# Optimization experiments

Measured on AMD Instinct MI355X. Metric: run time of the kernel, lower is better.

Reference implementation:

```python
import jax, jax.numpy as jnp
import numpy as np

H, D = 16, 64          # num_heads, head_dim
OUT = H * D            # out_dim = 1024
W1, W2 = 32, 32        # sliding windows
EPS_NORM = 1e-7
EPS_LN = 1e-5


def setup_inputs() -> dict:
    key = jax.random.key(0)
    ks = jax.random.split(key, 6)
    B, S, IN = 2, 2048, 1024
    x = jax.random.normal(ks[0], (B, S, IN), dtype=jnp.float32)
    scale = 0.02
    W_Q = jax.random.normal(ks[1], (IN, OUT), dtype=jnp.float32) * scale
    W_K = jax.random.normal(ks[2], (IN, OUT), dtype=jnp.float32) * scale
    W_V = jax.random.normal(ks[3], (IN, OUT), dtype=jnp.float32) * scale
    W_Kp = jax.random.normal(ks[4], (IN, OUT), dtype=jnp.float32) * scale
    W_O = jax.random.normal(ks[5], (OUT, OUT), dtype=jnp.float32) * scale
    ln_gamma = jnp.ones((OUT,), dtype=jnp.float32)
    ln_beta = jnp.zeros((OUT,), dtype=jnp.float32)
    return {"x": x, "W_Q": W_Q, "W_K": W_K, "W_V": W_V, "W_Kp": W_Kp,
            "W_O": W_O, "ln_gamma": ln_gamma, "ln_beta": ln_beta}


def _l2norm(t):
    return t / (jnp.linalg.norm(t, axis=-1, keepdims=True) + EPS_NORM)


def reference(x, W_Q, W_K, W_V, W_Kp, W_O, ln_gamma, ln_beta):
    B, S, _ = x.shape
    # projections -> (B, S, H, D)
    Q = _l2norm((x @ W_Q).reshape(B, S, H, D))
    K = _l2norm((x @ W_K).reshape(B, S, H, D))
    Kp = _l2norm((x @ W_Kp).reshape(B, S, H, D))
    V = (x @ W_V).reshape(B, S, H, D)
    # windowed keys/values (last w1/w2 positions, as in the PyTorch fallback)
    K_win = K[:, -W1:]
    Kp_win = Kp[:, -W2:]
    V_win = V[:, -W1:]
    Vp_win = V[:, -W2:]
    # triple product A_ijk = q.k.k' / sqrt(D) -> (B, S, H, w1, w2)
    A = jnp.einsum('bshd,bjhd,bkhd->bshjk', Q, K_win, Kp_win) / jnp.sqrt(jnp.float32(D))
    # causal window mask: allow j <= i + w1 - S and k <= i + w2 - S
    s_idx = jnp.arange(S)[:, None, None]
    j_idx = jnp.arange(W1)[None, :, None]
    k_idx = jnp.arange(W2)[None, None, :]
    mask = (j_idx > s_idx + (W1 - S)) | (k_idx > s_idx + (W2 - S))  # (S, w1, w2)
    neg_inf = jnp.float32(-jnp.inf)
    A = jnp.where(mask[None, :, None, :, :], neg_inf, A)
    # joint softmax over (j, k); fully-masked query rows produce zeros
    A_flat = A.reshape(B, S, H, W1 * W2)
    all_masked = jnp.all(A_flat == neg_inf, axis=-1, keepdims=True)
    A_safe = jnp.where(all_masked, 0.0, A_flat)
    P = jax.nn.softmax(A_safe, axis=-1)
    P = jnp.where(all_masked, 0.0, P).reshape(B, S, H, W1, W2)
    # value outer-product weighting (V' = V)
    Z = jnp.einsum('bshjk,bjhd,bkhd->bshd', P, V_win, Vp_win)
    out = Z.reshape(B, S, OUT) @ W_O
    out = out + x  # residual (shapes match)
    # LayerNorm
    mu = jnp.mean(out, axis=-1, keepdims=True)
    var = jnp.mean((out - mu) ** 2, axis=-1, keepdims=True)
    out = (out - mu) / jnp.sqrt(var + EPS_LN) * ln_gamma + ln_beta
    return out
```

## Files before the change

kernel.cpp:

```cpp
#include <hip/hip_runtime.h>
#include <math.h>


#define XS 68
#define WS 68

#define YP_STR   262144
#define NKS_P    8
#define ZF_OFF   (NKS_P * YP_STR)
#define DP_OFF   (ZF_OFF + 65536)
#define DP_STR   65536
#define NKS_W    16

__device__ __forceinline__ void ln_row(
    const float4* __restrict__ x4, const float4* __restrict__ g4,
    const float4* __restrict__ b4, float4* __restrict__ out4,
    int row, int lane) {
  float4 v[4];
  #pragma unroll
  for (int i = 0; i < 4; i++) v[i] = x4[row * 256 + i * 64 + lane];
  float sum = 0.f, ss = 0.f;
  #pragma unroll
  for (int i = 0; i < 4; i++) {
    sum += v[i].x + v[i].y + v[i].z + v[i].w;
    ss  += v[i].x * v[i].x + v[i].y * v[i].y + v[i].z * v[i].z + v[i].w * v[i].w;
  }
  #pragma unroll
  for (int off = 1; off < 64; off <<= 1) {
    sum += __shfl_xor(sum, off);
    ss  += __shfl_xor(ss, off);
  }
  float mu   = sum * (1.f / 1024.f);
  float rstd = rsqrtf(ss * (1.f / 1024.f) - mu * mu + 1e-5f);
  #pragma unroll
  for (int i = 0; i < 4; i++) {
    float4 g  = g4[i * 64 + lane];
    float4 be = b4[i * 64 + lane];
    float4 o;
    o.x = (v[i].x - mu) * rstd * g.x + be.x;
    o.y = (v[i].y - mu) * rstd * g.y + be.y;
    o.z = (v[i].z - mu) * rstd * g.z + be.z;
    o.w = (v[i].w - mu) * rstd * g.w + be.w;
    out4[row * 256 + i * 64 + lane] = o;
  }
}

__global__ __launch_bounds__(256, 4) void proj_ln_kernel(
    const float* __restrict__ x,
    const float* __restrict__ Wq, const float* __restrict__ Wk,
    const float* __restrict__ Wkp, const float* __restrict__ Wv,
    const float* __restrict__ gam, const float* __restrict__ bet,
    float* __restrict__ Y, float* __restrict__ out) {
  __shared__ float xs[64 * WS];
  __shared__ float wl[64 * WS];
  const int tid = threadIdx.x;
  const int bid = blockIdx.x;

  if (bid < 512) {
    const int cb   = bid & 63;
    const int ks   = bid >> 6;
    const int col0 = cb * 64;
    const int z    = cb >> 4;
    const int colz = col0 & 1023;
    const float* __restrict__ W =
        (z == 0) ? Wq : ((z == 1) ? Wk : ((z == 2) ? Wkp : Wv));
    const int tc = tid & 15, tr = tid >> 4;

    float acc[4][4];
    #pragma unroll
    for (int i = 0; i < 4; i++)
      #pragma unroll
      for (int j = 0; j < 4; j++) acc[i][j] = 0.f;

    for (int cc = 0; cc < 2; cc++) {
      const int kb = ks * 128 + cc * 64;
      #pragma unroll
      for (int i = 0; i < 4; i++) {
        int e = i * 256 + tid;
        int r = e >> 4, q = e & 15;
        int b = r >> 5, t = r & 31;
        float4 v = *(const float4*)(x + ((b * 2048 + 2016 + t) * 1024 + kb + q * 4));
        xs[(q * 4 + 0) * WS + r] = v.x;
        xs[(q * 4 + 1) * WS + r] = v.y;
        xs[(q * 4 + 2) * WS + r] = v.z;
        xs[(q * 4 + 3) * WS + r] = v.w;
        float4 w = *(const float4*)(W + (size_t)(kb + r) * 1024 + colz + q * 4);
        *(float4*)(wl + r * WS + q * 4) = w;
      }
      __syncthreads();

      #pragma unroll 8
      for (int kk = 0; kk < 64; kk++) {
        float4 xv = *(const float4*)(xs + kk * WS + tr * 4);
        float4 wv = *(const float4*)(wl + kk * WS + tc * 4);
        acc[0][0] = fmaf(xv.x, wv.x, acc[0][0]);
        acc[0][1] = fmaf(xv.x, wv.y, acc[0][1]);
        acc[0][2] = fmaf(xv.x, wv.z, acc[0][2]);
        acc[0][3] = fmaf(xv.x, wv.w, acc[0][3]);
        acc[1][0] = fmaf(xv.y, wv.x, acc[1][0]);
        acc[1][1] = fmaf(xv.y, wv.y, acc[1][1]);
        acc[1][2] = fmaf(xv.y, wv.z, acc[1][2]);
        acc[1][3] = fmaf(xv.y, wv.w, acc[1][3]);
        acc[2][0] = fmaf(xv.z, wv.x, acc[2][0]);
        acc[2][1] = fmaf(xv.z, wv.y, acc[2][1]);
        acc[2][2] = fmaf(xv.z, wv.z, acc[2][2]);
        acc[2][3] = fmaf(xv.z, wv.w, acc[2][3]);
        acc[3][0] = fmaf(xv.w, wv.x, acc[3][0]);
        acc[3][1] = fmaf(xv.w, wv.y, acc[3][1]);
        acc[3][2] = fmaf(xv.w, wv.z, acc[3][2]);
        acc[3][3] = fmaf(xv.w, wv.w, acc[3][3]);
      }
      __syncthreads();
    }

    float* __restrict__ Yo = Y + ks * YP_STR + col0;
    #pragma unroll
    for (int i = 0; i < 4; i++) {
      float4 o = make_float4(acc[i][0], acc[i][1], acc[i][2], acc[i][3]);
      *(float4*)(Yo + (tr * 4 + i) * 4096 + tc * 4) = o;
    }
  } else {
    const int wave = tid >> 6, lane = tid & 63;
    const int gw = (bid - 512) * 4 + wave;
    const float4* x4 = (const float4*)x;
    const float4* g4 = (const float4*)gam;
    const float4* b4 = (const float4*)bet;
    float4* out4 = (float4*)out;
    for (int idx = gw; idx < 4032; idx += 1792) {
      int row = (idx < 2016) ? idx : idx + 32;
      ln_row(x4, g4, b4, out4, row, lane);
    }
  }
}

__global__ __launch_bounds__(256) void attn_kernel(
    const float* __restrict__ Y, float* __restrict__ Zout) {
  __shared__ float Kn[32 * XS], Kp[32 * XS], Vs[32 * XS];
  __shared__ float Pt[4][32 * 33];
  __shared__ float qs[4][64];
  const int tid = threadIdx.x;
  const int wave = tid >> 6, lane = tid & 63;
  const int h = blockIdx.y, b = blockIdx.z;

  #pragma unroll
  for (int i = 0; i < 8; i++) {
    int e = i * 256 + tid;
    int row = e >> 6, d = e & 63;
    int src = (b * 32 + row) * 4096 + h * 64 + d;
    float kn = 0.f, kp = 0.f, vv = 0.f;
    #pragma unroll
    for (int p = 0; p < NKS_P; p++) {
      const float* Yp = Y + p * YP_STR + src;
      kn += Yp[1024]; kp += Yp[2048]; vv += Yp[3072];
    }
    Kn[row * XS + d] = kn; Kp[row * XS + d] = kp; Vs[row * XS + d] = vv;
  }
  __syncthreads();

  for (int rr = 0; rr < 8; rr++) {
    int row = wave * 8 + rr;
    float kv = Kn[row * XS + lane];
    float s2 = kv * kv;
    #pragma unroll
    for (int off = 1; off < 64; off <<= 1) s2 += __shfl_xor(s2, off);
    Kn[row * XS + lane] = kv * (1.f / (sqrtf(s2) + 1e-7f));
    float pv = Kp[row * XS + lane];
    float p2 = pv * pv;
    #pragma unroll
    for (int off = 1; off < 64; off <<= 1) p2 += __shfl_xor(p2, off);
    Kp[row * XS + lane] = pv * (1.f / (sqrtf(p2) + 1e-7f));
  }
  __syncthreads();

  const int m = blockIdx.x * 4 + wave;
  const int r = b * 32 + m;

  float q = 0.f;
  #pragma unroll
  for (int p = 0; p < NKS_P; p++) q += Y[p * YP_STR + r * 4096 + h * 64 + lane];
  float q2 = q * q;
  #pragma unroll
  for (int off = 1; off < 64; off <<= 1) q2 += __shfl_xor(q2, off);
  q *= (1.f / (sqrtf(q2) + 1e-7f));
  qs[wave][lane] = q;
  __builtin_amdgcn_wave_barrier();

  const int lj = lane >> 3, lk = lane & 7;
  float acc[4][4];
  #pragma unroll
  for (int a = 0; a < 4; a++)
    #pragma unroll
    for (int c = 0; c < 4; c++) acc[a][c] = 0.f;

  const float* qw = qs[wave];
  for (int dq = 0; dq < 16; dq++) {
    float4 q4 = *(const float4*)(qw + dq * 4);
    float4 t4[4], kp4[4];
    #pragma unroll
    for (int tj = 0; tj < 4; tj++) {
      float4 kv = *(const float4*)(Kn + (lj * 4 + tj) * XS + dq * 4);
      t4[tj].x = q4.x * kv.x; t4[tj].y = q4.y * kv.y;
      t4[tj].z = q4.z * kv.z; t4[tj].w = q4.w * kv.w;
    }
    #pragma unroll
    for (int tk = 0; tk < 4; tk++)
      kp4[tk] = *(const float4*)(Kp + (lk * 4 + tk) * XS + dq * 4);
    #pragma unroll
    for (int tj = 0; tj < 4; tj++)
      #pragma unroll
      for (int tk = 0; tk < 4; tk++)
        acc[tj][tk] += t4[tj].x * kp4[tk].x + t4[tj].y * kp4[tk].y
                     + t4[tj].z * kp4[tk].z + t4[tj].w * kp4[tk].w;
  }

  float amax = -1e30f;
  #pragma unroll
  for (int tj = 0; tj < 4; tj++)
    #pragma unroll
    for (int tk = 0; tk < 4; tk++) {
      int j = lj * 4 + tj, k = lk * 4 + tk;
      if (j <= m && k <= m) amax = fmaxf(amax, acc[tj][tk] * 0.125f);
    }
  #pragma unroll
  for (int off = 1; off < 64; off <<= 1) amax = fmaxf(amax, __shfl_xor(amax, off));

  float lsum = 0.f;
  float* ptw = Pt[wave];
  #pragma unroll
  for (int tj = 0; tj < 4; tj++)
    #pragma unroll
    for (int tk = 0; tk < 4; tk++) {
      int j = lj * 4 + tj, k = lk * 4 + tk;
      float e = 0.f;
      if (j <= m && k <= m) e = __expf(acc[tj][tk] * 0.125f - amax);
      lsum += e;
      ptw[k * 33 + j] = e;
    }
  #pragma unroll
  for (int off = 1; off < 64; off <<= 1) lsum += __shfl_xor(lsum, off);
  float inv = 1.f / lsum;
  __builtin_amdgcn_wave_barrier();

  float vreg[32];
  #pragma unroll
  for (int k = 0; k < 32; k++) vreg[k] = Vs[k * XS + lane];
  float zacc = 0.f;
  for (int k = 0; k <= m; k++) {
    float g = 0.f;
    #pragma unroll
    for (int j = 0; j < 32; j++) g += ptw[k * 33 + j] * vreg[j];
    zacc += g * vreg[k];
  }
  Zout[r * 1024 + h * 64 + lane] = zacc * inv;
}

__global__ __launch_bounds__(256, 4) void wo_kernel(
    const float* __restrict__ Zr, const float* __restrict__ Wo,
    float* __restrict__ Dp) {
  __shared__ float zs[64 * WS];
  __shared__ float wl[64 * WS];
  const int tid  = threadIdx.x;
  const int col0 = blockIdx.x * 64;
  const int ks   = blockIdx.y;
  const int kb   = ks * 64;
  const int tc = tid & 15, tr = tid >> 4;

  #pragma unroll
  for (int i = 0; i < 4; i++) {
    int e = i * 256 + tid;
    int r = e >> 4, q = e & 15;
    float4 v = *(const float4*)(Zr + r * 1024 + kb + q * 4);
    zs[(q * 4 + 0) * WS + r] = v.x;
    zs[(q * 4 + 1) * WS + r] = v.y;
    zs[(q * 4 + 2) * WS + r] = v.z;
    zs[(q * 4 + 3) * WS + r] = v.w;
    float4 w = *(const float4*)(Wo + (size_t)(kb + r) * 1024 + col0 + q * 4);
    *(float4*)(wl + r * WS + q * 4) = w;
  }
  __syncthreads();

  float acc[4][4];
  #pragma unroll
  for (int i = 0; i < 4; i++)
    #pragma unroll
    for (int j = 0; j < 4; j++) acc[i][j] = 0.f;

  #pragma unroll 8
  for (int kk = 0; kk < 64; kk++) {
    float4 xv = *(const float4*)(zs + kk * WS + tr * 4);
    float4 wv = *(const float4*)(wl + kk * WS + tc * 4);
    acc[0][0] = fmaf(xv.x, wv.x, acc[0][0]);
    acc[0][1] = fmaf(xv.x, wv.y, acc[0][1]);
    acc[0][2] = fmaf(xv.x, wv.z, acc[0][2]);
    acc[0][3] = fmaf(xv.x, wv.w, acc[0][3]);
    acc[1][0] = fmaf(xv.y, wv.x, acc[1][0]);
    acc[1][1] = fmaf(xv.y, wv.y, acc[1][1]);
    acc[1][2] = fmaf(xv.y, wv.z, acc[1][2]);
    acc[1][3] = fmaf(xv.y, wv.w, acc[1][3]);
    acc[2][0] = fmaf(xv.z, wv.x, acc[2][0]);
    acc[2][1] = fmaf(xv.z, wv.y, acc[2][1]);
    acc[2][2] = fmaf(xv.z, wv.z, acc[2][2]);
    acc[2][3] = fmaf(xv.z, wv.w, acc[2][3]);
    acc[3][0] = fmaf(xv.w, wv.x, acc[3][0]);
    acc[3][1] = fmaf(xv.w, wv.y, acc[3][1]);
    acc[3][2] = fmaf(xv.w, wv.z, acc[3][2]);
    acc[3][3] = fmaf(xv.w, wv.w, acc[3][3]);
  }

  float* __restrict__ D = Dp + ks * DP_STR + col0;
  #pragma unroll
  for (int i = 0; i < 4; i++) {
    float4 o = make_float4(acc[i][0], acc[i][1], acc[i][2], acc[i][3]);
    *(float4*)(D + (tr * 4 + i) * 1024 + tc * 4) = o;
  }
}

__global__ __launch_bounds__(256, 4) void ln_win_kernel(
    const float4* __restrict__ x4, const float4* __restrict__ dp4,
    const float4* __restrict__ g4, const float4* __restrict__ b4,
    float4* __restrict__ out4) {
  const int tid = threadIdx.x;
  const int wave = tid >> 6, lane = tid & 63;
  const int wr  = blockIdx.x * 4 + wave;
  const int row = (wr >> 5) * 2048 + 2016 + (wr & 31);

  float4 v[4];
  #pragma unroll
  for (int i = 0; i < 4; i++) v[i] = x4[row * 256 + i * 64 + lane];
  #pragma unroll
  for (int p = 0; p < NKS_W; p++) {
    #pragma unroll
    for (int i = 0; i < 4; i++) {
      float4 d = dp4[p * 16384 + wr * 256 + i * 64 + lane];
      v[i].x += d.x; v[i].y += d.y; v[i].z += d.z; v[i].w += d.w;
    }
  }
  float sum = 0.f, ss = 0.f;
  #pragma unroll
  for (int i = 0; i < 4; i++) {
    sum += v[i].x + v[i].y + v[i].z + v[i].w;
    ss  += v[i].x * v[i].x + v[i].y * v[i].y + v[i].z * v[i].z + v[i].w * v[i].w;
  }
  #pragma unroll
  for (int off = 1; off < 64; off <<= 1) {
    sum += __shfl_xor(sum, off);
    ss  += __shfl_xor(ss, off);
  }
  float mu   = sum * (1.f / 1024.f);
  float rstd = rsqrtf(ss * (1.f / 1024.f) - mu * mu + 1e-5f);

  #pragma unroll
  for (int i = 0; i < 4; i++) {
    float4 g = g4[i * 64 + lane];
    float4 be = b4[i * 64 + lane];
    float4 o;
    o.x = (v[i].x - mu) * rstd * g.x + be.x;
    o.y = (v[i].y - mu) * rstd * g.y + be.y;
    o.z = (v[i].z - mu) * rstd * g.z + be.z;
    o.w = (v[i].w - mu) * rstd * g.w + be.w;
    out4[row * 256 + i * 64 + lane] = o;
  }
}

extern "C" void kernel_launch(void* const* d_in, const int* in_sizes, int n_in,
                              void* d_out, int out_size, void* d_ws, size_t ws_size,
                              hipStream_t stream) {
  const float* x   = (const float*)d_in[0];
  const float* Wq  = (const float*)d_in[1];
  const float* Wk  = (const float*)d_in[2];
  const float* Wv  = (const float*)d_in[3];
  const float* Wkp = (const float*)d_in[4];
  const float* Wo  = (const float*)d_in[5];
  const float* gam = (const float*)d_in[6];
  const float* bet = (const float*)d_in[7];
  float* out = (float*)d_out;
  float* ws  = (float*)d_ws;

  hipLaunchKernelGGL(proj_ln_kernel, dim3(512 + 448), dim3(256), 0, stream,
                     x, Wq, Wk, Wkp, Wv, gam, bet, ws, out);
  hipLaunchKernelGGL(attn_kernel, dim3(8, 16, 2), dim3(256), 0, stream,
                     ws, ws + ZF_OFF);
  hipLaunchKernelGGL(wo_kernel, dim3(16, NKS_W), dim3(256), 0, stream,
                     ws + ZF_OFF, Wo, ws + DP_OFF);
  hipLaunchKernelGGL(ln_win_kernel, dim3(16), dim3(256), 0, stream,
                     (const float4*)x, (const float4*)(ws + DP_OFF),
                     (const float4*)gam, (const float4*)bet, (float4*)out);
}
```

Before: 128.8 us.

## Fuse attention, W_O projection and windowed LayerNorm into one kernel

Merges the attention, W_O matmul and window LayerNorm kernels into a single kernel. Each block multiplies its four Z rows for one head by that head's 64-row slice of W_O and writes per-head partial sums. The last block per row-group, found with an atomic counter and threadfence, sums the 16 partials and applies the residual and LayerNorm. This removes two kernel launches and the Z round trip through global memory. In exchange, W_O is read per block without shared-memory tiling, and the counters must be zeroed inside the projection kernel.

```diff
diff --git a/kernel.cpp b/kernel.cpp
--- a/kernel.cpp
+++ b/kernel.cpp
@@ -7,10 +7,9 @@
 
 #define YP_STR   262144
 #define NKS_P    8
-#define ZF_OFF   (NKS_P * YP_STR)
-#define DP_OFF   (ZF_OFF + 65536)
+#define DP_OFF   (NKS_P * YP_STR)
 #define DP_STR   65536
-#define NKS_W    16
+#define CNT_OFF  (DP_OFF + 16 * DP_STR)
 
 __device__ __forceinline__ void ln_row(
     const float4* __restrict__ x4, const float4* __restrict__ g4,
@@ -50,7 +49,7 @@
     const float* __restrict__ Wq, const float* __restrict__ Wk,
     const float* __restrict__ Wkp, const float* __restrict__ Wv,
     const float* __restrict__ gam, const float* __restrict__ bet,
-    float* __restrict__ Y, float* __restrict__ out) {
+    float* __restrict__ Y, float* __restrict__ out, int* __restrict__ cnt) {
   __shared__ float xs[64 * WS];
   __shared__ float wl[64 * WS];
   const int tid = threadIdx.x;
@@ -120,6 +119,7 @@
       *(float4*)(Yo + (tr * 4 + i) * 4096 + tc * 4) = o;
     }
   } else {
+    if (bid == 512 && tid < 16) cnt[tid] = 0;
     const int wave = tid >> 6, lane = tid & 63;
     const int gw = (bid - 512) * 4 + wave;
     const float4* x4 = (const float4*)x;
@@ -133,14 +133,19 @@
   }
 }
 
-__global__ __launch_bounds__(256) void attn_kernel(
-    const float* __restrict__ Y, float* __restrict__ Zout) {
+__global__ __launch_bounds__(256) void attn_wo_kernel(
+    const float* __restrict__ Y, const float* __restrict__ Wo,
+    const float* __restrict__ x, const float* __restrict__ gam,
+    const float* __restrict__ bet, float* __restrict__ Dp,
+    int* __restrict__ cnt, float* __restrict__ out) {
   __shared__ float Kn[32 * XS], Kp[32 * XS], Vs[32 * XS];
   __shared__ float Pt[4][32 * 33];
   __shared__ float qs[4][64];
+  __shared__ float Zs[4][64];
+  __shared__ int done_flag;
   const int tid = threadIdx.x;
   const int wave = tid >> 6, lane = tid & 63;
-  const int h = blockIdx.y, b = blockIdx.z;
+  const int mb = blockIdx.x, h = blockIdx.y, b = blockIdx.z;
 
   #pragma unroll
   for (int i = 0; i < 8; i++) {
@@ -172,7 +177,7 @@
   }
   __syncthreads();
 
-  const int m = blockIdx.x * 4 + wave;
+  const int m = mb * 4 + wave;
   const int r = b * 32 + m;
 
   float q = 0.f;
@@ -251,84 +256,59 @@
     for (int j = 0; j < 32; j++) g += ptw[k * 33 + j] * vreg[j];
     zacc += g * vreg[k];
   }
-  Zout[r * 1024 + h * 64 + lane] = zacc * inv;
-}
-
-__global__ __launch_bounds__(256, 4) void wo_kernel(
-    const float* __restrict__ Zr, const float* __restrict__ Wo,
-    float* __restrict__ Dp) {
-  __shared__ float zs[64 * WS];
-  __shared__ float wl[64 * WS];
-  const int tid  = threadIdx.x;
-  const int col0 = blockIdx.x * 64;
-  const int ks   = blockIdx.y;
-  const int kb   = ks * 64;
-  const int tc = tid & 15, tr = tid >> 4;
-
-  #pragma unroll
-  for (int i = 0; i < 4; i++) {
-    int e = i * 256 + tid;
-    int r = e >> 4, q = e & 15;
-    float4 v = *(const float4*)(Zr + r * 1024 + kb + q * 4);
-    zs[(q * 4 + 0) * WS + r] = v.x;
-    zs[(q * 4 + 1) * WS + r] = v.y;
-    zs[(q * 4 + 2) * WS + r] = v.z;
-    zs[(q * 4 + 3) * WS + r] = v.w;
-    float4 w = *(const float4*)(Wo + (size_t)(kb + r) * 1024 + col0 + q * 4);
-    *(float4*)(wl + r * WS + q * 4) = w;
-  }
-  __syncthreads();
-
-  float acc[4][4];
+  Zs[wave][lane] = zacc * inv;
+  __syncthreads();
+
+  float wacc[4][4];
   #pragma unroll
   for (int i = 0; i < 4; i++)
     #pragma unroll
-    for (int j = 0; j < 4; j++) acc[i][j] = 0.f;
-
-  #pragma unroll 8
-  for (int kk = 0; kk < 64; kk++) {
-    float4 xv = *(const float4*)(zs + kk * WS + tr * 4);
-    float4 wv = *(const float4*)(wl + kk * WS + tc * 4);
-    acc[0][0] = fmaf(xv.x, wv.x, acc[0][0]);
-    acc[0][1] = fmaf(xv.x, wv.y, acc[0][1]);
-    acc[0][2] = fmaf(xv.x, wv.z, acc[0][2]);
-    acc[0][3] = fmaf(xv.x, wv.w, acc[0][3]);
-    acc[1][0] = fmaf(xv.y, wv.x, acc[1][0]);
-    acc[1][1] = fmaf(xv.y, wv.y, acc[1][1]);
-    acc[1][2] = fmaf(xv.y, wv.z, acc[1][2]);
-    acc[1][3] = fmaf(xv.y, wv.w, acc[1][3]);
-    acc[2][0] = fmaf(xv.z, wv.x, acc[2][0]);
-    acc[2][1] = fmaf(xv.z, wv.y, acc[2][1]);
-    acc[2][2] = fmaf(xv.z, wv.z, acc[2][2]);
-    acc[2][3] = fmaf(xv.z, wv.w, acc[2][3]);
-    acc[3][0] = fmaf(xv.w, wv.x, acc[3][0]);
-    acc[3][1] = fmaf(xv.w, wv.y, acc[3][1]);
-    acc[3][2] = fmaf(xv.w, wv.z, acc[3][2]);
-    acc[3][3] = fmaf(xv.w, wv.w, acc[3][3]);
-  }
-
-  float* __restrict__ D = Dp + ks * DP_STR + col0;
-  #pragma unroll
-  for (int i = 0; i < 4; i++) {
-    float4 o = make_float4(acc[i][0], acc[i][1], acc[i][2], acc[i][3]);
-    *(float4*)(D + (tr * 4 + i) * 1024 + tc * 4) = o;
-  }
-}
-
-__global__ __launch_bounds__(256, 4) void ln_win_kernel(
-    const float4* __restrict__ x4, const float4* __restrict__ dp4,
-    const float4* __restrict__ g4, const float4* __restrict__ b4,
-    float4* __restrict__ out4) {
-  const int tid = threadIdx.x;
-  const int wave = tid >> 6, lane = tid & 63;
-  const int wr  = blockIdx.x * 4 + wave;
-  const int row = (wr >> 5) * 2048 + 2016 + (wr & 31);
+    for (int j = 0; j < 4; j++) wacc[i][j] = 0.f;
+
+  const float* __restrict__ WoS = Wo + (size_t)h * 65536 + tid * 4;
+  #pragma unroll 4
+  for (int k = 0; k < 64; k++) {
+    float4 wv = *(const float4*)(WoS + (size_t)k * 1024);
+    #pragma unroll
+    for (int rr = 0; rr < 4; rr++) {
+      float zz = Zs[rr][k];
+      wacc[rr][0] = fmaf(zz, wv.x, wacc[rr][0]);
+      wacc[rr][1] = fmaf(zz, wv.y, wacc[rr][1]);
+      wacc[rr][2] = fmaf(zz, wv.z, wacc[rr][2]);
+      wacc[rr][3] = fmaf(zz, wv.w, wacc[rr][3]);
+    }
+  }
+  const int r0 = b * 32 + mb * 4;
+  float* __restrict__ D = Dp + h * DP_STR;
+  #pragma unroll
+  for (int rr = 0; rr < 4; rr++) {
+    float4 o = make_float4(wacc[rr][0], wacc[rr][1], wacc[rr][2], wacc[rr][3]);
+    *(float4*)(D + (size_t)(r0 + rr) * 1024 + tid * 4) = o;
+  }
+
+  __threadfence();
+  __syncthreads();
+  if (tid == 0) {
+    int old = atomicAdd(cnt + (b * 8 + mb), 1);
+    done_flag = (old == 15) ? 1 : 0;
+  }
+  __syncthreads();
+  if (!done_flag) return;
+  __threadfence();
+
+  const int wr  = r0 + wave;
+  const int row = b * 2048 + 2016 + mb * 4 + wave;
+  const float4* x4  = (const float4*)x;
+  const float4* dp4 = (const float4*)Dp;
+  const float4* g4  = (const float4*)gam;
+  const float4* b4  = (const float4*)bet;
+  float4* out4 = (float4*)out;
 
   float4 v[4];
   #pragma unroll
   for (int i = 0; i < 4; i++) v[i] = x4[row * 256 + i * 64 + lane];
   #pragma unroll
-  for (int p = 0; p < NKS_W; p++) {
+  for (int p = 0; p < 16; p++) {
     #pragma unroll
     for (int i = 0; i < 4; i++) {
       float4 d = dp4[p * 16384 + wr * 256 + i * 64 + lane];
@@ -348,10 +328,9 @@
   }
   float mu   = sum * (1.f / 1024.f);
   float rstd = rsqrtf(ss * (1.f / 1024.f) - mu * mu + 1e-5f);
-
   #pragma unroll
   for (int i = 0; i < 4; i++) {
-    float4 g = g4[i * 64 + lane];
+    float4 g  = g4[i * 64 + lane];
     float4 be = b4[i * 64 + lane];
     float4 o;
     o.x = (v[i].x - mu) * rstd * g.x + be.x;
@@ -375,14 +354,10 @@
   const float* bet = (const float*)d_in[7];
   float* out = (float*)d_out;
   float* ws  = (float*)d_ws;
+  int*   cnt = (int*)(ws + CNT_OFF);
 
   hipLaunchKernelGGL(proj_ln_kernel, dim3(512 + 448), dim3(256), 0, stream,
-                     x, Wq, Wk, Wkp, Wv, gam, bet, ws, out);
-  hipLaunchKernelGGL(attn_kernel, dim3(8, 16, 2), dim3(256), 0, stream,
-                     ws, ws + ZF_OFF);
-  hipLaunchKernelGGL(wo_kernel, dim3(16, NKS_W), dim3(256), 0, stream,
-                     ws + ZF_OFF, Wo, ws + DP_OFF);
-  hipLaunchKernelGGL(ln_win_kernel, dim3(16), dim3(256), 0, stream,
-                     (const float4*)x, (const float4*)(ws + DP_OFF),
-                     (const float4*)gam, (const float4*)bet, (float4*)out);
+                     x, Wq, Wk, Wkp, Wv, gam, bet, ws, out, cnt);
+  hipLaunchKernelGGL(attn_wo_kernel, dim3(8, 16, 2), dim3(256), 0, stream,
+                     ws, Wo, x, gam, bet, ws + DP_OFF, cnt, out);
 }
```

Result: slower. 160.4 us (+24.5%).
